# Optimization experiments

Hardware: AMD Instinct MI355X
Metric: run time of the kernel (lower is better)

The kernel has to match this reference:

```python
import jax, jax.numpy as jnp
import numpy as np

N_NODES = 100000
FEAT = 256
HID = 128
REL = 2
BATCH = 20000
K = 10  # filtersize


def setup_inputs() -> dict:
    key = jax.random.key(0)
    k1, k2, k3, k4, k5 = jax.random.split(key, 5)
    nodes = jax.random.randint(k1, (BATCH,), 0, N_NODES)
    neigh_idx = jax.random.randint(k2, (REL, BATCH, K), 0, N_NODES)
    features = jax.random.normal(k3, (N_NODES, FEAT), dtype=jnp.float32)
    W_stc = jax.random.normal(k4, (REL, FEAT, HID), dtype=jnp.float32) * (1.0 / np.sqrt(FEAT))
    W_det = jax.random.normal(k5, (FEAT + REL * HID, HID), dtype=jnp.float32) * (1.0 / np.sqrt(FEAT + REL * HID))
    return {"nodes": nodes, "neigh_idx": neigh_idx, "features": features,
            "W_stc": W_stc, "W_det": W_det}


def reference(nodes, neigh_idx, features, W_stc, W_det):
    # self features: irregular gather [B, F]
    self_feats = features[nodes]
    # per-relation neighbor gather [R, B, K, F] -> mean over sampled neighbors [R, B, F]
    neigh_mean = features[neigh_idx].mean(axis=2)
    # STC layer projection to hidden per relation: [R, B, H]
    neigh_h = jnp.einsum('rbf,rfh->rbh', neigh_mean, W_stc)
    # concat self feats with each relation's neighbor embedding: [B, F + R*H]
    combined = jnp.concatenate(
        [self_feats, jnp.moveaxis(neigh_h, 0, 1).reshape(neigh_h.shape[1], -1)], axis=1)
    # linear + relu (dropout_flag=False -> no dropout)
    return jax.nn.relu(combined @ W_det)
```

## Files before the change

kernel.cpp:

```cpp
#include <hip/hip_runtime.h>
#include <hip/hip_bf16.h>

#define N_NODES 100000
#define FEAT    256
#define HID     128
#define REL     2
#define BATCH   20000
#define KNEI    10

#define APAD    8
#define AROW    (768 + APAD)

typedef short bf16x8 __attribute__((ext_vector_type(8)));
typedef float f32x4  __attribute__((ext_vector_type(4)));

__device__ __forceinline__ unsigned short f2bf(float x) {
    union { float f; unsigned u; } v; v.f = x;
    unsigned r = v.u + 0x7fffu + ((v.u >> 16) & 1u);
    return (unsigned short)(r >> 16);
}

__device__ __forceinline__ ushort4 pack4(float a, float b, float c, float d) {
    ushort4 p; p.x = f2bf(a); p.y = f2bf(b); p.z = f2bf(c); p.w = f2bf(d);
    return p;
}

__device__ __forceinline__ size_t bsw_index(int k, int n) {
    int kt = k >> 5, j = k & 7, hi = (k >> 3) & 3;
    int lane = hi * 16 + (n & 15), nt = n >> 4;
    return ((size_t)(kt * 8 + nt) * 64 + lane) * 8 + j;
}

__global__ __launch_bounds__(256) void prep_B(const float* __restrict__ W_stc,
                                              const float* __restrict__ W_det,
                                              unsigned short* __restrict__ Bsw) {
    const int blk = blockIdx.x;
    const int tid = threadIdx.x;
    if (blk < 32) {
        const int rel   = blk >> 4;
        const int fbase = (blk & 15) * 16;
        const int n     = tid & 127;
        const int fh    = tid >> 7;
        const float* wd = W_det + (size_t)(256 + rel * HID) * HID + n;
        #pragma unroll
        for (int fo = 0; fo < 8; ++fo) {
            const int f = fbase + fh * 8 + fo;
            const float* ws = W_stc + (size_t)(rel * FEAT + f) * HID;
            float acc = 0.f;
            #pragma unroll 8
            for (int j2 = 0; j2 < HID; ++j2) acc += ws[j2] * wd[(size_t)j2 * HID];
            const int k = 256 + rel * 256 + f;
            Bsw[bsw_index(k, n)] = f2bf(acc);
        }
    } else {
        const int base = (blk - 32) * 16384;
        #pragma unroll 4
        for (int i = 0; i < 64; ++i) {
            const int idx = base + i * 256 + tid;
            const int k = idx >> 7, n = idx & 127;
            Bsw[bsw_index(k, n)] = f2bf(W_det[idx]);
        }
    }
}

__global__ __launch_bounds__(256, 4) void fused(const int* __restrict__ nodes,
                                                const int* __restrict__ neigh_idx,
                                                const float* __restrict__ features,
                                                const unsigned short* __restrict__ Bsw,
                                                float* __restrict__ out) {
    __shared__ unsigned short As[16 * AROW];

    const int blk  = blockIdx.x;
    const int w    = threadIdx.x >> 6;
    const int lane = threadIdx.x & 63;
    const float4* F4 = (const float4*)features;
    const float inv = 1.0f / (float)KNEI;

    #pragma unroll
    for (int e = 0; e < 4; ++e) {
        const int m = w * 4 + e;
        const int b = blk * 16 + m;
        const int self = nodes[b];
        const int* i0 = neigh_idx + (size_t)b * KNEI;
        const int* i1 = neigh_idx + (size_t)(BATCH + b) * KNEI;

        float4 sf = F4[(size_t)self * 64 + lane];
        float4 s0 = make_float4(0.f, 0.f, 0.f, 0.f);
        float4 s1 = make_float4(0.f, 0.f, 0.f, 0.f);
        #pragma unroll
        for (int k = 0; k < KNEI; ++k) {
            float4 v = F4[(size_t)i0[k] * 64 + lane];
            s0.x += v.x; s0.y += v.y; s0.z += v.z; s0.w += v.w;
        }
        #pragma unroll
        for (int k = 0; k < KNEI; ++k) {
            float4 v = F4[(size_t)i1[k] * 64 + lane];
            s1.x += v.x; s1.y += v.y; s1.z += v.z; s1.w += v.w;
        }
        ushort4* row = (ushort4*)(As + m * AROW);
        row[lane]       = pack4(sf.x, sf.y, sf.z, sf.w);
        row[64 + lane]  = pack4(s0.x * inv, s0.y * inv, s0.z * inv, s0.w * inv);
        row[128 + lane] = pack4(s1.x * inv, s1.y * inv, s1.z * inv, s1.w * inv);
    }
    __syncthreads();

    const int quad = lane >> 4;
    const int l16  = lane & 15;
    const unsigned short* a_base = As + l16 * AROW + quad * 8;

    f32x4 acc0 = (f32x4){0.f, 0.f, 0.f, 0.f};
    f32x4 acc1 = (f32x4){0.f, 0.f, 0.f, 0.f};
    const int nt0 = w, nt1 = w + 4;

    #pragma unroll
    for (int kt = 0; kt < 24; ++kt) {
        bf16x8 a = *(const bf16x8*)(a_base + kt * 32);
        const unsigned short* bk = Bsw + ((size_t)(kt * 8) * 64 + lane) * 8;
        bf16x8 b0 = *(const bf16x8*)(bk + (size_t)nt0 * 64 * 8);
        bf16x8 b1 = *(const bf16x8*)(bk + (size_t)nt1 * 64 * 8);
        acc0 = __builtin_amdgcn_mfma_f32_16x16x32_bf16(a, b0, acc0, 0, 0, 0);
        acc1 = __builtin_amdgcn_mfma_f32_16x16x32_bf16(a, b1, acc1, 0, 0, 0);
    }

    float* orow = out + (size_t)(blk * 16) * HID;
    #pragma unroll
    for (int r = 0; r < 4; ++r) {
        const int row = quad * 4 + r;
        float v0 = acc0[r];
        float v1 = acc1[r];
        orow[(size_t)row * HID + nt0 * 16 + l16] = v0 > 0.f ? v0 : 0.f;
        orow[(size_t)row * HID + nt1 * 16 + l16] = v1 > 0.f ? v1 : 0.f;
    }
}

extern "C" void kernel_launch(void* const* d_in, const int* in_sizes, int n_in,
                              void* d_out, int out_size, void* d_ws, size_t ws_size,
                              hipStream_t stream) {
    const int*   nodes     = (const int*)d_in[0];
    const int*   neigh_idx = (const int*)d_in[1];
    const float* features  = (const float*)d_in[2];
    const float* W_stc     = (const float*)d_in[3];
    const float* W_det     = (const float*)d_in[4];
    float* out = (float*)d_out;

    unsigned short* Bsw = (unsigned short*)d_ws;

    prep_B<<<34, 256, 0, stream>>>(W_stc, W_det, Bsw);
    fused<<<BATCH / 16, 256, 0, stream>>>(nodes, neigh_idx, features, Bsw, out);
}
```

Baseline: 231.6 us.

## Project all node features first, then gather and sum projected rows

Reorders the computation so the projection runs before the gather. A dense GEMM computes H = features @ [W_self | W_stc0·W_det0/K | W_stc1·W_det1/K] for every node and stores it in bf16. A second kernel then gathers the needed 128-column slice per node and relation, sums the slices and applies ReLU. This replaces 21 random 1 KB feature-row gathers per batch item with 256-byte gathers of projected rows, plus one streaming pass over all features. The costs are a GEMM over all 100k nodes, a 77 MB intermediate write, and extra rounding because H is stored in bf16 before summation.

```diff
diff --git a/kernel.cpp b/kernel.cpp
--- a/kernel.cpp
+++ b/kernel.cpp
@@ -8,8 +8,10 @@
 #define BATCH   20000
 #define KNEI    10
 
-#define APAD    8
-#define AROW    (768 + APAD)
+#define NCOL 384
+#define NT   24
+#define KT   8
+#define ASTRIDE 264
 
 typedef short bf16x8 __attribute__((ext_vector_type(8)));
 typedef float f32x4  __attribute__((ext_vector_type(4)));
@@ -28,10 +30,10 @@
 __device__ __forceinline__ size_t bsw_index(int k, int n) {
     int kt = k >> 5, j = k & 7, hi = (k >> 3) & 3;
     int lane = hi * 16 + (n & 15), nt = n >> 4;
-    return ((size_t)(kt * 8 + nt) * 64 + lane) * 8 + j;
+    return ((size_t)(kt * NT + nt) * 64 + lane) * 8 + j;
 }
 
-__global__ __launch_bounds__(256) void prep_B(const float* __restrict__ W_stc,
+__global__ __launch_bounds__(256) void prep_W(const float* __restrict__ W_stc,
                                               const float* __restrict__ W_det,
                                               unsigned short* __restrict__ Bsw) {
     const int blk = blockIdx.x;
@@ -42,6 +44,7 @@
         const int n     = tid & 127;
         const int fh    = tid >> 7;
         const float* wd = W_det + (size_t)(256 + rel * HID) * HID + n;
+        const float scale = 1.0f / (float)KNEI;
         #pragma unroll
         for (int fo = 0; fo < 8; ++fo) {
             const int f = fbase + fh * 8 + fo;
@@ -49,8 +52,7 @@
             float acc = 0.f;
             #pragma unroll 8
             for (int j2 = 0; j2 < HID; ++j2) acc += ws[j2] * wd[(size_t)j2 * HID];
-            const int k = 256 + rel * 256 + f;
-            Bsw[bsw_index(k, n)] = f2bf(acc);
+            Bsw[bsw_index(f, 128 + rel * 128 + n)] = f2bf(acc * scale);
         }
     } else {
         const int base = (blk - 32) * 16384;
@@ -63,74 +65,98 @@
     }
 }
 
-__global__ __launch_bounds__(256, 4) void fused(const int* __restrict__ nodes,
-                                                const int* __restrict__ neigh_idx,
-                                                const float* __restrict__ features,
-                                                const unsigned short* __restrict__ Bsw,
-                                                float* __restrict__ out) {
-    __shared__ unsigned short As[16 * AROW];
+__global__ __launch_bounds__(256, 2) void gemm_H(const float* __restrict__ features,
+                                                 const unsigned short* __restrict__ Bsw,
+                                                 unsigned short* __restrict__ H) {
+    __shared__ unsigned short Asm[64 * ASTRIDE];
 
-    const int blk  = blockIdx.x;
-    const int w    = threadIdx.x >> 6;
-    const int lane = threadIdx.x & 63;
+    const int row0 = blockIdx.x * 64;
+    const int tid  = threadIdx.x;
     const float4* F4 = (const float4*)features;
-    const float inv = 1.0f / (float)KNEI;
 
     #pragma unroll
-    for (int e = 0; e < 4; ++e) {
-        const int m = w * 4 + e;
-        const int b = blk * 16 + m;
-        const int self = nodes[b];
-        const int* i0 = neigh_idx + (size_t)b * KNEI;
-        const int* i1 = neigh_idx + (size_t)(BATCH + b) * KNEI;
-
-        float4 sf = F4[(size_t)self * 64 + lane];
-        float4 s0 = make_float4(0.f, 0.f, 0.f, 0.f);
-        float4 s1 = make_float4(0.f, 0.f, 0.f, 0.f);
-        #pragma unroll
-        for (int k = 0; k < KNEI; ++k) {
-            float4 v = F4[(size_t)i0[k] * 64 + lane];
-            s0.x += v.x; s0.y += v.y; s0.z += v.z; s0.w += v.w;
-        }
-        #pragma unroll
-        for (int k = 0; k < KNEI; ++k) {
-            float4 v = F4[(size_t)i1[k] * 64 + lane];
-            s1.x += v.x; s1.y += v.y; s1.z += v.z; s1.w += v.w;
-        }
-        ushort4* row = (ushort4*)(As + m * AROW);
-        row[lane]       = pack4(sf.x, sf.y, sf.z, sf.w);
-        row[64 + lane]  = pack4(s0.x * inv, s0.y * inv, s0.z * inv, s0.w * inv);
-        row[128 + lane] = pack4(s1.x * inv, s1.y * inv, s1.z * inv, s1.w * inv);
+    for (int i = 0; i < 16; ++i) {
+        const int idx = i * 256 + tid;
+        const int r   = idx >> 6;
+        const int c4  = idx & 63;
+        int rg = row0 + r;
+        if (rg >= N_NODES) rg = N_NODES - 1;
+        float4 v = F4[(size_t)rg * 64 + c4];
+        *(ushort4*)(Asm + r * ASTRIDE + c4 * 4) = pack4(v.x, v.y, v.z, v.w);
     }
     __syncthreads();
 
+    const int w    = tid >> 6;
+    const int lane = tid & 63;
     const int quad = lane >> 4;
     const int l16  = lane & 15;
-    const unsigned short* a_base = As + l16 * AROW + quad * 8;
+    const unsigned short* a_base = Asm + (w * 16 + l16) * ASTRIDE + quad * 8;
 
-    f32x4 acc0 = (f32x4){0.f, 0.f, 0.f, 0.f};
-    f32x4 acc1 = (f32x4){0.f, 0.f, 0.f, 0.f};
-    const int nt0 = w, nt1 = w + 4;
+    f32x4 acc[NT];
+    #pragma unroll
+    for (int nt = 0; nt < NT; ++nt) acc[nt] = (f32x4){0.f, 0.f, 0.f, 0.f};
 
     #pragma unroll
-    for (int kt = 0; kt < 24; ++kt) {
+    for (int kt = 0; kt < KT; ++kt) {
         bf16x8 a = *(const bf16x8*)(a_base + kt * 32);
-        const unsigned short* bk = Bsw + ((size_t)(kt * 8) * 64 + lane) * 8;
-        bf16x8 b0 = *(const bf16x8*)(bk + (size_t)nt0 * 64 * 8);
-        bf16x8 b1 = *(const bf16x8*)(bk + (size_t)nt1 * 64 * 8);
-        acc0 = __builtin_amdgcn_mfma_f32_16x16x32_bf16(a, b0, acc0, 0, 0, 0);
-        acc1 = __builtin_amdgcn_mfma_f32_16x16x32_bf16(a, b1, acc1, 0, 0, 0);
+        const unsigned short* bk = Bsw + ((size_t)kt * NT * 64 + lane) * 8;
+        #pragma unroll
+        for (int nt = 0; nt < NT; ++nt) {
+            bf16x8 bfr = *(const bf16x8*)(bk + (size_t)nt * 64 * 8);
+            acc[nt] = __builtin_amdgcn_mfma_f32_16x16x32_bf16(a, bfr, acc[nt], 0, 0, 0);
+        }
     }
 
-    float* orow = out + (size_t)(blk * 16) * HID;
+    const int rbase = row0 + w * 16 + quad * 4;
     #pragma unroll
     for (int r = 0; r < 4; ++r) {
-        const int row = quad * 4 + r;
-        float v0 = acc0[r];
-        float v1 = acc1[r];
-        orow[(size_t)row * HID + nt0 * 16 + l16] = v0 > 0.f ? v0 : 0.f;
-        orow[(size_t)row * HID + nt1 * 16 + l16] = v1 > 0.f ? v1 : 0.f;
+        const int row = rbase + r;
+        if (row < N_NODES) {
+            unsigned short* hrow = H + (size_t)row * NCOL + l16;
+            #pragma unroll
+            for (int nt = 0; nt < NT; ++nt)
+                hrow[nt * 16] = f2bf(acc[nt][r]);
+        }
     }
+}
+
+__global__ __launch_bounds__(256) void gather_out(const int* __restrict__ nodes,
+                                                  const int* __restrict__ neigh_idx,
+                                                  const unsigned short* __restrict__ H,
+                                                  float* __restrict__ out) {
+    const int w    = threadIdx.x >> 6;
+    const int lane = threadIdx.x & 63;
+    const int b    = blockIdx.x * 4 + w;
+    if (b >= BATCH) return;
+
+    const unsigned* Hd = (const unsigned*)H;
+    const int self = nodes[b];
+    const int* i0 = neigh_idx + (size_t)b * KNEI;
+    const int* i1 = neigh_idx + (size_t)(BATCH + b) * KNEI;
+
+    union { unsigned u; float f; } lo, hi;
+    unsigned u = Hd[(size_t)self * 192 + lane];
+    lo.u = u << 16;
+    hi.u = u & 0xffff0000u;
+    float a0 = lo.f, a1 = hi.f;
+
+    #pragma unroll
+    for (int k = 0; k < KNEI; ++k) {
+        unsigned v = Hd[(size_t)i0[k] * 192 + 64 + lane];
+        lo.u = v << 16; hi.u = v & 0xffff0000u;
+        a0 += lo.f; a1 += hi.f;
+    }
+    #pragma unroll
+    for (int k = 0; k < KNEI; ++k) {
+        unsigned v = Hd[(size_t)i1[k] * 192 + 128 + lane];
+        lo.u = v << 16; hi.u = v & 0xffff0000u;
+        a0 += lo.f; a1 += hi.f;
+    }
+
+    float2 r;
+    r.x = a0 > 0.f ? a0 : 0.f;
+    r.y = a1 > 0.f ? a1 : 0.f;
+    ((float2*)(out + (size_t)b * HID))[lane] = r;
 }
 
 extern "C" void kernel_launch(void* const* d_in, const int* in_sizes, int n_in,
@@ -144,7 +170,9 @@
     float* out = (float*)d_out;
 
     unsigned short* Bsw = (unsigned short*)d_ws;
+    unsigned short* H   = (unsigned short*)((char*)d_ws + 256 * 1024);
 
-    prep_B<<<34, 256, 0, stream>>>(W_stc, W_det, Bsw);
-    fused<<<BATCH / 16, 256, 0, stream>>>(nodes, neigh_idx, features, Bsw, out);
+    prep_W<<<34, 256, 0, stream>>>(W_stc, W_det, Bsw);
+    gemm_H<<<(N_NODES + 63) / 64, 256, 0, stream>>>(features, Bsw, H);
+    gather_out<<<(BATCH + 3) / 4, 256, 0, stream>>>(nodes, neigh_idx, H, out);
 }
```

New measurement: 348.8 us. 50.6% more time.
